# Optimization experiments

Measured on AMD Instinct MI355X. Metric: run time of the kernel, lower is better.

## Reference

```python
import jax, jax.numpy as jnp
import numpy as np

I = 4  # input size
H = 4  # hidden size


def setup_inputs() -> dict:
    key = jax.random.key(0)
    ks = jax.random.split(key, 7)
    T, B = 2048, 8192
    s = 1.0 / np.sqrt(H)  # torch LSTM/Linear init scale
    x = jax.random.normal(ks[0], (T, B, I), dtype=jnp.float32)
    w_ih = jax.random.uniform(ks[1], (4 * H, I), minval=-s, maxval=s, dtype=jnp.float32)
    w_hh = jax.random.uniform(ks[2], (4 * H, H), minval=-s, maxval=s, dtype=jnp.float32)
    b_ih = jax.random.uniform(ks[3], (4 * H,), minval=-s, maxval=s, dtype=jnp.float32)
    b_hh = jax.random.uniform(ks[4], (4 * H,), minval=-s, maxval=s, dtype=jnp.float32)
    w_lin = jax.random.uniform(ks[5], (1, H), minval=-0.5, maxval=0.5, dtype=jnp.float32)
    b_lin = jax.random.uniform(ks[6], (1,), minval=-0.5, maxval=0.5, dtype=jnp.float32)
    return {"x": x, "w_ih": w_ih, "w_hh": w_hh, "b_ih": b_ih, "b_hh": b_hh,
            "w_lin": w_lin, "b_lin": b_lin}


def _lstm_scan(x, w_ih, w_hh, b_ih, b_hh):
    # x: (T, B, I). PyTorch gate order: i, f, g, o.
    T, B, _ = x.shape
    b = b_ih + b_hh  # (4H,)
    # Precompute input projections for all timesteps: (T, B, 4H)
    xg = jnp.einsum('tbi,gi->tbg', x, w_ih) + b

    def step(carry, xg_t):
        h, c = carry  # (B, H) each
        gates = xg_t + h @ w_hh.T  # (B, 4H)
        i, f, g, o = jnp.split(gates, 4, axis=-1)
        i = jax.nn.sigmoid(i)
        f = jax.nn.sigmoid(f)
        g = jnp.tanh(g)
        o = jax.nn.sigmoid(o)
        c = f * c + i * g
        h = o * jnp.tanh(c)
        return (h, c), h

    h0 = jnp.zeros((B, H), dtype=x.dtype)
    c0 = jnp.zeros((B, H), dtype=x.dtype)
    _, hs = jax.lax.scan(step, (h0, c0), xg)
    return hs  # (T, B, H)


def reference(x, w_ih, w_hh, b_ih, b_hh, w_lin, b_lin):
    hs = _lstm_scan(x, w_ih, w_hh, b_ih, b_hh)           # (T, B, H)
    out = jnp.einsum('tbh,oh->tbo', hs, w_lin) + b_lin   # (T, B, 1)
    return jax.nn.sigmoid(out)
```

## Files before the change

### kernel.cpp

```cpp
#include <hip/hip_runtime.h>

#define T_DIM 2048
#define B_DIM 8192
#define PH    256
#define SPH   8

__device__ __forceinline__ float dpp_qxor1(float v) {
  int i = __float_as_int(v);
  return __int_as_float(__builtin_amdgcn_update_dpp(i, i, 0xB1, 0xF, 0xF, false));
}
__device__ __forceinline__ float dpp_qxor2(float v) {
  int i = __float_as_int(v);
  return __int_as_float(__builtin_amdgcn_update_dpp(i, i, 0x4E, 0xF, 0xF, false));
}
__device__ __forceinline__ float dpp_qxor3(float v) {
  int i = __float_as_int(v);
  return __int_as_float(__builtin_amdgcn_update_dpp(i, i, 0x1B, 0xF, 0xF, false));
}
__device__ __forceinline__ float dpp_hmirror(float v) {
  int i = __float_as_int(v);
  return __int_as_float(__builtin_amdgcn_update_dpp(i, i, 0x141, 0xF, 0xF, false));
}

__global__ __launch_bounds__(512) void lstm_pc_kernel(
    const float* __restrict__ x,
    const float* __restrict__ w_ih, const float* __restrict__ w_hh,
    const float* __restrict__ b_ih, const float* __restrict__ b_hh,
    const float* __restrict__ w_lin, const float* __restrict__ b_lin,
    float* __restrict__ out)
{
  __shared__ float xaBuf[2][4][64][18];
  __shared__ float hnBuf[2][4][64][9];

  const int tid  = threadIdx.x;
  const int wid  = tid >> 6;
  const int lane = tid & 63;
  const int pair = wid & 3;

  const float L2E = 1.4426950408889634f;
  const float cm2 = -2.0f * L2E;

  const int l = lane & 7;
  const int half1 = (l >> 2) & 1;
  const int e = (l & 3) ^ (half1 ? 3 : 0);
  const int grp = lane >> 3;
  const int rA = half1 * 4 + e;
  const int rB = 8 + half1 * 4 + e;
  const float sclA = -L2E;
  const float sclB = half1 ? -L2E : -2.0f * L2E;

  if (wid < 4) {
    __builtin_amdgcn_s_setprio(1);
    float whhA[4], whhB[4];
    #pragma unroll
    for (int k = 0; k < 4; ++k) {
      const int j = e ^ k;
      whhA[k] = sclA * w_hh[rA * 4 + j];
      whhB[k] = sclB * w_hh[rB * 4 + j];
    }
    const float sB = half1 ? 1.0f : 2.0f * cm2;
    const float oB = half1 ? 0.0f : -cm2;
    float ct = 0.0f, h0 = 0.0f, h1 = 0.0f, h2 = 0.0f, h3 = 0.0f;

    __syncthreads();

    for (int p = 0; p < PH; ++p) {
      const int d = p & 1;
      float xaA[SPH], xaB[SPH];
      #pragma unroll
      for (int k = 0; k < SPH; ++k) {
        xaA[k] = xaBuf[d][pair][lane][2 * k];
        xaB[k] = xaBuf[d][pair][lane][2 * k + 1];
      }
      #pragma unroll
      for (int k = 0; k < SPH; ++k) {
        float uA = fmaf(whhA[0], h0, xaA[k]);
        uA = fmaf(whhA[1], h1, uA);
        uA = fmaf(whhA[2], h2, uA);
        uA = fmaf(whhA[3], h3, uA);
        float uB = fmaf(whhB[0], h0, xaB[k]);
        uB = fmaf(whhB[1], h1, uB);
        uB = fmaf(whhB[2], h2, uB);
        uB = fmaf(whhB[3], h3, uB);
        const float aA = __builtin_amdgcn_rcpf(1.0f + __builtin_amdgcn_exp2f(uA));
        const float yB = __builtin_amdgcn_rcpf(1.0f + __builtin_amdgcn_exp2f(uB));
        const float aB = fmaf(sB, yB, oB);
        const float Z = half1 ? aA : aA * aB;
        const float W = dpp_hmirror(Z);
        const float F = half1 ? Z : W;
        const float P = half1 ? W : Z;
        ct = fmaf(F, ct, P);
        const float zc = __builtin_amdgcn_exp2f(ct);
        const float rc = __builtin_amdgcn_rcpf(1.0f + zc);
        const float Ox = dpp_hmirror(aB);
        const float ov = half1 ? aB : Ox;
        const float tc = fmaf(2.0f, rc, -1.0f);
        const float hn = ov * tc;
        h0 = hn;
        h1 = dpp_qxor1(hn);
        h2 = dpp_qxor2(hn);
        h3 = dpp_qxor3(hn);
        hnBuf[d][pair][lane][k] = hn;
      }
      __syncthreads();
    }
  } else {
    const int b = blockIdx.x * 32 + pair * 8 + grp;
    float wihA[4], wihB[4];
    #pragma unroll
    for (int k = 0; k < 4; ++k) {
      const int j = e ^ k;
      wihA[k] = sclA * w_ih[rA * 4 + j];
      wihB[k] = sclB * w_ih[rB * 4 + j];
    }
    const float biasA = sclA * (b_ih[rA] + b_hh[rA]);
    const float biasB = sclB * (b_ih[rB] + b_hh[rB]);
    const int og = lane & 7, oj = lane >> 3;
    const int ob = blockIdx.x * 32 + pair * 8 + og;
    float wl[4];
    #pragma unroll
    for (int j = 0; j < 4; ++j) wl[j] = -L2E * w_lin[j];
    const float blin = -L2E * b_lin[0];

    const int XS = B_DIM * 4;
    const int xoff = b * 4 + e;

    float xc[SPH], xn[SPH];

    auto load8 = [&](float (&dst)[SPH], int ph) {
      const int base = xoff + ((ph & (PH - 1)) * SPH) * XS;
      #pragma unroll
      for (int k = 0; k < SPH; ++k) dst[k] = x[base + k * XS];
    };
    auto projWrite = [&](const float (&xr)[SPH], int dd) {
      #pragma unroll
      for (int k = 0; k < SPH; ++k) {
        const float xe = xr[k];
        const float x1 = dpp_qxor1(xe);
        const float x2 = dpp_qxor2(xe);
        const float x3 = dpp_qxor3(xe);
        float a = fmaf(wihA[0], xe, biasA);
        a = fmaf(wihA[1], x1, a);
        a = fmaf(wihA[2], x2, a);
        a = fmaf(wihA[3], x3, a);
        float bb = fmaf(wihB[0], xe, biasB);
        bb = fmaf(wihB[1], x1, bb);
        bb = fmaf(wihB[2], x2, bb);
        bb = fmaf(wihB[3], x3, bb);
        xaBuf[dd][pair][lane][2 * k]     = a;
        xaBuf[dd][pair][lane][2 * k + 1] = bb;
      }
    };
    auto headStore = [&](int p, int dh) {
      const float v0 = hnBuf[dh][pair][og * 8 + 0][oj];
      const float v1 = hnBuf[dh][pair][og * 8 + 1][oj];
      const float v2 = hnBuf[dh][pair][og * 8 + 2][oj];
      const float v3 = hnBuf[dh][pair][og * 8 + 3][oj];
      float m = fmaf(wl[0], v0, blin);
      m = fmaf(wl[1], v1, m);
      m = fmaf(wl[2], v2, m);
      m = fmaf(wl[3], v3, m);
      const float o = __builtin_amdgcn_rcpf(1.0f + __builtin_amdgcn_exp2f(m));
      out[(size_t)(p * SPH + oj) * B_DIM + ob] = o;
    };

    load8(xc, 0);
    projWrite(xc, 0);
    load8(xn, 1);
    __syncthreads();

    for (int pp = 0; pp < PH; pp += 2) {
      projWrite(xn, 1);
      load8(xc, pp + 2);
      if (pp > 0) headStore(pp - 1, 1);
      __syncthreads();
      projWrite(xc, 0);
      load8(xn, pp + 3);
      headStore(pp, 0);
      __syncthreads();
    }
    headStore(PH - 1, 1);
  }
}

extern "C" void kernel_launch(void* const* d_in, const int* in_sizes, int n_in,
                              void* d_out, int out_size, void* d_ws, size_t ws_size,
                              hipStream_t stream) {
  const float* x     = (const float*)d_in[0];
  const float* w_ih  = (const float*)d_in[1];
  const float* w_hh  = (const float*)d_in[2];
  const float* b_ih  = (const float*)d_in[3];
  const float* b_hh  = (const float*)d_in[4];
  const float* w_lin = (const float*)d_in[5];
  const float* b_lin = (const float*)d_in[6];
  float* out = (float*)d_out;

  dim3 block(512);
  dim3 grid(B_DIM / 32);
  hipLaunchKernelGGL(lstm_pc_kernel, grid, block, 0, stream,
                     x, w_ih, w_hh, b_ih, b_hh, w_lin, b_lin, out);
}
```

Measured before the change: 248.9 us.

## Fuse output head into recurrent waves and merge gate reciprocals

Moves the linear+sigmoid output head from the producer waves into the recurrent waves. The head of step t is computed from the already-broadcast h registers during step t+1, and its exp/rcp reuses the slot the tanh(c) path uses on the other half of the lanes. This removes the hnBuf shared-memory round trip and its LDS writes. Gate math now shares one reciprocal per product (i*g via a combined denominator), the stored projection pairs become float2 for wider LDS access, and ct is clamped before exp2. In exchange the latency-critical recurrent loop gains extra FMAs, a select and a global store per step, which could lengthen the serial chain.

```diff
diff --git a/kernel.cpp b/kernel.cpp
--- a/kernel.cpp
+++ b/kernel.cpp
@@ -22,15 +22,14 @@
   return __int_as_float(__builtin_amdgcn_update_dpp(i, i, 0x141, 0xF, 0xF, false));
 }
 
-__global__ __launch_bounds__(512) void lstm_pc_kernel(
+__global__ __launch_bounds__(512) void lstm_fused_kernel(
     const float* __restrict__ x,
     const float* __restrict__ w_ih, const float* __restrict__ w_hh,
     const float* __restrict__ b_ih, const float* __restrict__ b_hh,
     const float* __restrict__ w_lin, const float* __restrict__ b_lin,
     float* __restrict__ out)
 {
-  __shared__ float xaBuf[2][4][64][18];
-  __shared__ float hnBuf[2][4][64][9];
+  __shared__ float2 xaBuf[2][4][64][9];
 
   const int tid  = threadIdx.x;
   const int wid  = tid >> 6;
@@ -51,16 +50,21 @@
 
   if (wid < 4) {
     __builtin_amdgcn_s_setprio(1);
-    float whhA[4], whhB[4];
+    float whhA[4], whhB[4], wl[4];
     #pragma unroll
     for (int k = 0; k < 4; ++k) {
       const int j = e ^ k;
       whhA[k] = sclA * w_hh[rA * 4 + j];
       whhB[k] = sclB * w_hh[rB * 4 + j];
-    }
-    const float sB = half1 ? 1.0f : 2.0f * cm2;
-    const float oB = half1 ? 0.0f : -cm2;
-    float ct = 0.0f, h0 = 0.0f, h1 = 0.0f, h2 = 0.0f, h3 = 0.0f;
+      wl[k]   = -L2E * w_lin[j];
+    }
+    const float blinS = -L2E * b_lin[0];
+    const float nmA = half1 ? 0.0f : -cm2;
+    const float nmB = half1 ? 1.0f :  cm2;
+    const float q2 = half1 ? -1.0f : 0.0f;
+
+    const int b = blockIdx.x * 32 + pair * 8 + grp;
+    float ct = 0.0f, h0 = 0.0f, h1v = 0.0f, h2v = 0.0f, h3v = 0.0f;
 
     __syncthreads();
 
@@ -69,41 +73,70 @@
       float xaA[SPH], xaB[SPH];
       #pragma unroll
       for (int k = 0; k < SPH; ++k) {
-        xaA[k] = xaBuf[d][pair][lane][2 * k];
-        xaB[k] = xaBuf[d][pair][lane][2 * k + 1];
+        const float2 v = xaBuf[d][pair][lane][k];
+        xaA[k] = v.x;
+        xaB[k] = v.y;
       }
       #pragma unroll
       for (int k = 0; k < SPH; ++k) {
         float uA = fmaf(whhA[0], h0, xaA[k]);
-        uA = fmaf(whhA[1], h1, uA);
-        uA = fmaf(whhA[2], h2, uA);
-        uA = fmaf(whhA[3], h3, uA);
+        uA = fmaf(whhA[1], h1v, uA);
+        uA = fmaf(whhA[2], h2v, uA);
+        uA = fmaf(whhA[3], h3v, uA);
         float uB = fmaf(whhB[0], h0, xaB[k]);
-        uB = fmaf(whhB[1], h1, uB);
-        uB = fmaf(whhB[2], h2, uB);
-        uB = fmaf(whhB[3], h3, uB);
-        const float aA = __builtin_amdgcn_rcpf(1.0f + __builtin_amdgcn_exp2f(uA));
-        const float yB = __builtin_amdgcn_rcpf(1.0f + __builtin_amdgcn_exp2f(uB));
-        const float aB = fmaf(sB, yB, oB);
-        const float Z = half1 ? aA : aA * aB;
+        uB = fmaf(whhB[1], h1v, uB);
+        uB = fmaf(whhB[2], h2v, uB);
+        uB = fmaf(whhB[3], h3v, uB);
+
+        float m = fmaf(wl[0], h0, blinS);
+        m = fmaf(wl[1], h1v, m);
+        m = fmaf(wl[2], h2v, m);
+        m = fmaf(wl[3], h3v, m);
+
+        const float EA = __builtin_amdgcn_exp2f(uA);
+        const float EB = __builtin_amdgcn_exp2f(uB);
+        const float dA = 1.0f + EA;
+        const float dB = 1.0f + EB;
+        const float s1   = half1 ? 1.0f : dB;
+        const float den1 = dA * s1;
+        const float r1   = __builtin_amdgcn_rcpf(den1);
+        const float nm1  = fmaf(nmA, EB, nmB);
+        const float Z    = nm1 * r1;
         const float W = dpp_hmirror(Z);
         const float F = half1 ? Z : W;
         const float P = half1 ? W : Z;
         ct = fmaf(F, ct, P);
-        const float zc = __builtin_amdgcn_exp2f(ct);
-        const float rc = __builtin_amdgcn_rcpf(1.0f + zc);
-        const float Ox = dpp_hmirror(aB);
-        const float ov = half1 ? aB : Ox;
-        const float tc = fmaf(2.0f, rc, -1.0f);
-        const float hn = ov * tc;
-        h0 = hn;
-        h1 = dpp_qxor1(hn);
-        h2 = dpp_qxor2(hn);
-        h3 = dpp_qxor3(hn);
-        hnBuf[d][pair][lane][k] = hn;
+
+        const float ctc  = fminf(ct, 120.0f);
+        const float src  = half1 ? ctc : m;
+        const float E2   = __builtin_amdgcn_exp2f(src);
+        const float d2   = 1.0f + E2;
+        const float s2   = half1 ? dB : 1.0f;
+        const float den2 = d2 * s2;
+        const float r2   = __builtin_amdgcn_rcpf(den2);
+        const float nm2  = fmaf(q2, E2, 1.0f);
+        const float w    = nm2 * r2;
+        const float hm   = dpp_hmirror(w);
+        const float hn   = half1 ? w : hm;
+
+        if (p > 0 || k > 0) {
+          if (l == 0) out[(size_t)(p * SPH + k - 1) * B_DIM + b] = w;
+        }
+
+        h0  = hn;
+        h1v = dpp_qxor1(hn);
+        h2v = dpp_qxor2(hn);
+        h3v = dpp_qxor3(hn);
       }
       __syncthreads();
     }
+    float m = fmaf(wl[0], h0, blinS);
+    m = fmaf(wl[1], h1v, m);
+    m = fmaf(wl[2], h2v, m);
+    m = fmaf(wl[3], h3v, m);
+    const float Et = __builtin_amdgcn_exp2f(m);
+    const float ot = __builtin_amdgcn_rcpf(1.0f + Et);
+    if (l == 0) out[(size_t)(T_DIM - 1) * B_DIM + b] = ot;
   } else {
     const int b = blockIdx.x * 32 + pair * 8 + grp;
     float wihA[4], wihB[4];
@@ -115,12 +148,6 @@
     }
     const float biasA = sclA * (b_ih[rA] + b_hh[rA]);
     const float biasB = sclB * (b_ih[rB] + b_hh[rB]);
-    const int og = lane & 7, oj = lane >> 3;
-    const int ob = blockIdx.x * 32 + pair * 8 + og;
-    float wl[4];
-    #pragma unroll
-    for (int j = 0; j < 4; ++j) wl[j] = -L2E * w_lin[j];
-    const float blin = -L2E * b_lin[0];
 
     const int XS = B_DIM * 4;
     const int xoff = b * 4 + e;
@@ -147,21 +174,8 @@
         bb = fmaf(wihB[1], x1, bb);
         bb = fmaf(wihB[2], x2, bb);
         bb = fmaf(wihB[3], x3, bb);
-        xaBuf[dd][pair][lane][2 * k]     = a;
-        xaBuf[dd][pair][lane][2 * k + 1] = bb;
+        xaBuf[dd][pair][lane][k] = make_float2(a, bb);
       }
-    };
-    auto headStore = [&](int p, int dh) {
-      const float v0 = hnBuf[dh][pair][og * 8 + 0][oj];
-      const float v1 = hnBuf[dh][pair][og * 8 + 1][oj];
-      const float v2 = hnBuf[dh][pair][og * 8 + 2][oj];
-      const float v3 = hnBuf[dh][pair][og * 8 + 3][oj];
-      float m = fmaf(wl[0], v0, blin);
-      m = fmaf(wl[1], v1, m);
-      m = fmaf(wl[2], v2, m);
-      m = fmaf(wl[3], v3, m);
-      const float o = __builtin_amdgcn_rcpf(1.0f + __builtin_amdgcn_exp2f(m));
-      out[(size_t)(p * SPH + oj) * B_DIM + ob] = o;
     };
 
     load8(xc, 0);
@@ -172,14 +186,11 @@
     for (int pp = 0; pp < PH; pp += 2) {
       projWrite(xn, 1);
       load8(xc, pp + 2);
-      if (pp > 0) headStore(pp - 1, 1);
       __syncthreads();
       projWrite(xc, 0);
       load8(xn, pp + 3);
-      headStore(pp, 0);
       __syncthreads();
     }
-    headStore(PH - 1, 1);
   }
 }
 
@@ -197,6 +208,6 @@
 
   dim3 block(512);
   dim3 grid(B_DIM / 32);
-  hipLaunchKernelGGL(lstm_pc_kernel, grid, block, 0, stream,
+  hipLaunchKernelGGL(lstm_fused_kernel, grid, block, 0, stream,
                      x, w_ih, w_hh, b_ih, b_hh, w_lin, b_lin, out);
 }
```

Result: slower. 274.1 us (+10.1%).
